# Performance work log

Measured on AMD Instinct MI355X. Metric: run time of the kernel, lower is better.

## Reference

```python
import jax, jax.numpy as jnp
import numpy as np

B, S, D, H = 2, 2048, 1024, 16
HD = D // H               # head_dim = input_size / num_heads
STEPS = 1                 # update_steps_max extra Hopfield update steps
LN_EPS = 1e-5
SCALING = 1.0 / np.sqrt(HD)  # beta = 1/sqrt(head_dim)


def layernorm(x, g, b):
    m = x.mean(-1, keepdims=True)
    v = ((x - m) ** 2).mean(-1, keepdims=True)
    return (x - m) * jax.lax.rsqrt(v + LN_EPS) * g + b


def setup_inputs() -> dict:
    key = jax.random.key(0)
    ks = jax.random.split(key, 9)
    s = 0.02
    f32 = jnp.float32
    return {
        "data": jax.random.normal(ks[0], (B, S, D), f32),
        # affine LayerNorm params (stored / state / projection patterns)
        "g_k": jnp.ones((D,), f32), "b_k": jnp.zeros((D,), f32),
        "g_q": jnp.ones((D,), f32), "b_q": jnp.zeros((D,), f32),
        "g_v": jnp.ones((D,), f32), "b_v": jnp.zeros((D,), f32),
        # in-projections (q/k/v) and out-projection of HopfieldCore
        "Wq": jax.random.normal(ks[1], (D, D), f32) * s, "bq": jnp.zeros((D,), f32),
        "Wk": jax.random.normal(ks[2], (D, D), f32) * s, "bk": jnp.zeros((D,), f32),
        "Wv": jax.random.normal(ks[3], (D, D), f32) * s, "bv": jnp.zeros((D,), f32),
        "Wo": jax.random.normal(ks[4], (D, D), f32) * s, "bo": jnp.zeros((D,), f32),
    }


def reference(data, g_k, b_k, g_q, b_q, g_v, b_v,
              Wq, bq, Wk, bk, Wv, bv, Wo, bo):
    # single input tensor used as stored / state / projection pattern
    xk = layernorm(data, g_k, b_k)   # stored pattern  -> keys
    xq = layernorm(data, g_q, b_q)   # state pattern   -> queries
    xv = layernorm(data, g_v, b_v)   # pattern proj    -> values

    split = lambda t: t.reshape(B, S, H, HD).transpose(0, 2, 1, 3)  # [B,H,S,HD]
    q = split(xq @ Wq + bq)
    k = split(xk @ Wk + bk)
    v = split(xv @ Wv + bv)

    def assoc(q):  # xi = softmax(beta * q K^T)
        return jax.nn.softmax(
            jnp.einsum('bhqd,bhkd->bhqk', q, k) * SCALING, axis=-1)

    xi = assoc(q)
    for _ in range(STEPS):           # iterative Hopfield update: q <- xi K
        q = jnp.einsum('bhqk,bhkd->bhqd', xi, k)
        xi = assoc(q)

    out = jnp.einsum('bhqk,bhkd->bhqd', xi, v)        # retrieve with values
    out = out.transpose(0, 2, 1, 3).reshape(B, S, D)  # merge heads
    return out @ Wo + bo
```

## Files before the change

### kernel.cpp

```cpp
#include <hip/hip_runtime.h>
#include <hip/hip_bf16.h>

#define B_  2
#define S_  2048
#define D_  1024
#define H_  16
#define HD_ 64
#define M_  4096


typedef __attribute__((ext_vector_type(8))) short short8;
typedef __attribute__((ext_vector_type(4))) float f32x4;
typedef __attribute__((ext_vector_type(16))) float f32x16;

#define CE_ 0.1803368801111204f

typedef __attribute__((address_space(1))) const unsigned GU;
typedef __attribute__((address_space(3))) unsigned LU;
static __device__ __forceinline__ void glds16(const void* g, void* l){
  __builtin_amdgcn_global_load_lds((GU*)g, (LU*)l, 16, 0, 0);
}

static __device__ __forceinline__ unsigned short f2bfc(float f){
  union{float f; unsigned u;} c; c.f = f;
  return (unsigned short)((c.u + 0x8000u) >> 16);
}
static __device__ __forceinline__ unsigned pk2bf(float a, float b){
  union{float f; unsigned u;} ca, cb; ca.f=a; cb.f=b;
  return __builtin_amdgcn_perm(cb.u + 0x8000u, ca.u + 0x8000u, 0x07060302u);
}
static __device__ __forceinline__ unsigned pk2bft(float a, float b){
  union{float f; unsigned u;} ca, cb; ca.f=a; cb.f=b;
  return __builtin_amdgcn_perm(cb.u, ca.u, 0x07060302u);
}
static __device__ __forceinline__ short8 mk8(unsigned x0, unsigned x1,
                                             unsigned x2, unsigned x3){
  union{ unsigned u[4]; short8 s; } t;
  t.u[0]=x0; t.u[1]=x1; t.u[2]=x2; t.u[3]=x3; return t.s;
}
static __device__ __forceinline__ void plswap(unsigned &x, unsigned &y){
  auto r = __builtin_amdgcn_permlane32_swap(x, y, false, false);
  x = (unsigned)r[0]; y = (unsigned)r[1];
}

__global__ __launch_bounds__(256) void prep_kernel(
  const float* __restrict__ data,
  const float* __restrict__ Wq, const float* __restrict__ Wk,
  const float* __restrict__ Wv, const float* __restrict__ Wo,
  const float* __restrict__ gq, const float* __restrict__ gk, const float* __restrict__ gv,
  const float* __restrict__ blq, const float* __restrict__ blk, const float* __restrict__ blv,
  const float* __restrict__ bpq, const float* __restrict__ bpk, const float* __restrict__ bpv,
  unsigned short* __restrict__ WT, unsigned short* __restrict__ xhat,
  float* __restrict__ bf)
{
  __shared__ unsigned short tile[64][72];
  __shared__ float red[4][64];
  int bid = blockIdx.x, t = threadIdx.x;
  if (bid < 1024){
    int z = bid >> 8, rem = bid & 255;
    int k0 = (rem>>4)*64, n0 = (rem&15)*64;
    const float* W = (z==0)?Wq:(z==1)?Wk:(z==2)?Wv:Wo;
    const float* g = (z==0)?gq:(z==1)?gk:(z==2)?gv:(const float*)0;
    unsigned short* out = WT + ((size_t)z<<20);
    {
      int kr = t>>2, c16 = (t&3)*16;
      float gs = g ? g[k0+kr]*((z==0)?CE_:1.0f) : 1.0f;
      const float* src = W + (size_t)(k0+kr)*D_ + n0 + c16;
      float4 w0 = *(const float4*)(src);
      float4 w1 = *(const float4*)(src+4);
      float4 w2 = *(const float4*)(src+8);
      float4 w3 = *(const float4*)(src+12);
      unsigned* tp = (unsigned*)&tile[kr][c16];
      tp[0]=pk2bf(w0.x*gs,w0.y*gs); tp[1]=pk2bf(w0.z*gs,w0.w*gs);
      tp[2]=pk2bf(w1.x*gs,w1.y*gs); tp[3]=pk2bf(w1.z*gs,w1.w*gs);
      tp[4]=pk2bf(w2.x*gs,w2.y*gs); tp[5]=pk2bf(w2.z*gs,w2.w*gs);
      tp[6]=pk2bf(w3.x*gs,w3.y*gs); tp[7]=pk2bf(w3.z*gs,w3.w*gs);
    }
    __syncthreads();
    {
      int nr = t>>2, kc = (t&3)*16;
      union { uint4 v[2]; unsigned short u[16]; } st;
      #pragma unroll
      for (int i=0;i<16;i++) st.u[i] = tile[kc+i][nr];
      unsigned short* dst = out + (size_t)(n0+nr)*D_ + k0 + kc;
      *(uint4*)(dst)     = st.v[0];
      *(uint4*)(dst + 8) = st.v[1];
    }
  } else if (bid < 2048){
    int row = (bid-1024)*4 + (t>>6);
    int l = t & 63;
    const float4* xr = (const float4*)(data + (size_t)row*D_);
    float4 v[4];
    float s = 0.f, ss = 0.f;
    #pragma unroll
    for (int i=0;i<4;i++){
      v[i] = xr[l + 64*i];
      s  += v[i].x+v[i].y+v[i].z+v[i].w;
      ss += v[i].x*v[i].x+v[i].y*v[i].y+v[i].z*v[i].z+v[i].w*v[i].w;
    }
    #pragma unroll
    for (int m=1;m<64;m<<=1){ s += __shfl_xor(s, m, 64); ss += __shfl_xor(ss, m, 64); }
    float me = s*(1.0f/D_);
    float var = ss*(1.0f/D_) - me*me;
    float rs = rsqrtf(var + 1e-5f);
    float nm = -me*rs;
    unsigned short* xo = xhat + (size_t)row*D_;
    #pragma unroll
    for (int i=0;i<4;i++){
      uint2 pk;
      pk.x = pk2bf(fmaf(v[i].x,rs,nm), fmaf(v[i].y,rs,nm));
      pk.y = pk2bf(fmaf(v[i].z,rs,nm), fmaf(v[i].w,rs,nm));
      *(uint2*)(xo + 4*l + 256*i) = pk;
    }
  } else {
    int idx = bid - 2048;
    int z = idx >> 4, xb = idx & 15;
    const float* W  = (z==0)?Wq:(z==1)?Wk:Wv;
    const float* bl = (z==0)?blq:(z==1)?blk:blv;
    const float* bp = (z==0)?bpq:(z==1)?bpk:bpv;
    int nl = t & 63, kg = t >> 6;
    int n = xb*64 + nl;
    float acc = 0.f;
    for (int k = kg*256; k < (kg+1)*256; k++)
      acc += bl[k] * W[(size_t)k*D_ + n];
    red[kg][nl] = acc;
    __syncthreads();
    if (t < 64){
      int nn = xb*64 + t;
      float v = red[0][t]+red[1][t]+red[2][t]+red[3][t] + bp[nn];
      bf[z*D_ + nn] = (z==0) ? v*CE_ : v;
    }
  }
}

__global__ __launch_bounds__(256) void gemm_qkv(
  const unsigned short* __restrict__ xhat,
  const unsigned short* __restrict__ WT,
  const float* __restrict__ biasf,
  unsigned short* __restrict__ qv, unsigned short* __restrict__ kb,
  unsigned short* __restrict__ kT, unsigned short* __restrict__ vT)
{
  int z = blockIdx.z;
  const unsigned short* Bt = WT + ((size_t)z<<20);
  const float* bias = biasf + z*D_;
  unsigned short* oN = (z==0)?qv:(z==1)?kb:(unsigned short*)0;
  unsigned short* oT = (z==0)?(unsigned short*)0:(z==1)?kT:vT;

  __shared__ __align__(16) unsigned short As[128*32];
  __shared__ __align__(16) unsigned short Bs[128*32];
  int tid = threadIdx.x, w = tid>>6, l = tid&63;
  int m0 = blockIdx.x*128, n0 = blockIdx.y*128;
  int wr = (w>>1)*64, wc = (w&1)*64;
  int lr = l&15, qd = l>>4;

  const unsigned short* gA = xhat + (size_t)(m0 + w*32 + (l>>2))*D_ + (l&3)*8;
  const unsigned short* gB = Bt   + (size_t)(n0 + w*32 + (l>>2))*D_ + (l&3)*8;
  unsigned short* lA0 = &As[(w*32)*32];
  unsigned short* lA1 = &As[(w*32+16)*32];
  unsigned short* lB0 = &Bs[(w*32)*32];
  unsigned short* lB1 = &Bs[(w*32+16)*32];

  const f32x4 fz = {0.f,0.f,0.f,0.f};
  f32x4 acc[4][4];
  #pragma unroll
  for (int i=0;i<4;i++)
    #pragma unroll
    for (int j=0;j<4;j++) acc[i][j] = fz;

  for (int kk=0; kk<D_; kk+=32){
    __syncthreads();
    glds16(gA + kk,                 lA0);
    glds16(gA + kk + (size_t)16*D_, lA1);
    glds16(gB + kk,                 lB0);
    glds16(gB + kk + (size_t)16*D_, lB1);
    __syncthreads();
    short8 af[4], bfr[4];
    #pragma unroll
    for (int i=0;i<4;i++) af[i]  = *(const short8*)(As + (wr + i*16 + lr)*32 + qd*8);
    #pragma unroll
    for (int j=0;j<4;j++) bfr[j] = *(const short8*)(Bs + (wc + j*16 + lr)*32 + qd*8);
    #pragma unroll
    for (int i=0;i<4;i++)
      #pragma unroll
      for (int j=0;j<4;j++)
        acc[i][j] = __builtin_amdgcn_mfma_f32_16x16x32_bf16(af[i], bfr[j], acc[i][j], 0, 0, 0);
  }

  #pragma unroll
  for (int j=0;j<4;j++){
    int n = n0 + wc + j*16 + lr;
    float bias_n = bias[n];
    #pragma unroll
    for (int i=0;i<4;i++){
      int mb = m0 + wr + i*16 + qd*4;
      float v0 = acc[i][j][0] + bias_n;
      float v1 = acc[i][j][1] + bias_n;
      float v2 = acc[i][j][2] + bias_n;
      float v3 = acc[i][j][3] + bias_n;
      if (oN){
        oN[(size_t)(mb+0)*D_ + n] = f2bfc(v0);
        oN[(size_t)(mb+1)*D_ + n] = f2bfc(v1);
        oN[(size_t)(mb+2)*D_ + n] = f2bfc(v2);
        oN[(size_t)(mb+3)*D_ + n] = f2bfc(v3);
      }
      if (oT){
        int bb = mb >> 11, sI = mb & (S_-1);
        int hh = n >> 6,  dd = n & 63;
        uint2 pk; pk.x = pk2bf(v0, v1); pk.y = pk2bf(v2, v3);
        *(uint2*)(oT + (size_t)((bb*H_ + hh)*HD_ + dd)*S_ + sI) = pk;
      }
    }
  }
}

__global__ __launch_bounds__(256) void gemm_out(
  const unsigned short* __restrict__ A,
  const unsigned short* __restrict__ Bt,
  const float* __restrict__ bo,
  float* __restrict__ Cf)
{
  __shared__ __align__(16) unsigned short As[128*32];
  __shared__ __align__(16) unsigned short Bs[128*32];
  int tid = threadIdx.x, w = tid>>6, l = tid&63;
  int m0 = blockIdx.x*128, n0 = blockIdx.y*128;
  int wr = (w>>1)*64, wc = (w&1)*64;
  int lr = l&15, qd = l>>4;

  const unsigned short* gA = A  + (size_t)(m0 + w*32 + (l>>2))*D_ + (l&3)*8;
  const unsigned short* gB = Bt + (size_t)(n0 + w*32 + (l>>2))*D_ + (l&3)*8;
  unsigned short* lA0 = &As[(w*32)*32];
  unsigned short* lA1 = &As[(w*32+16)*32];
  unsigned short* lB0 = &Bs[(w*32)*32];
  unsigned short* lB1 = &Bs[(w*32+16)*32];

  const f32x4 fz = {0.f,0.f,0.f,0.f};
  f32x4 acc[4][4];
  #pragma unroll
  for (int i=0;i<4;i++)
    #pragma unroll
    for (int j=0;j<4;j++) acc[i][j] = fz;

  for (int kk=0; kk<D_; kk+=32){
    __syncthreads();
    glds16(gA + kk,                 lA0);
    glds16(gA + kk + (size_t)16*D_, lA1);
    glds16(gB + kk,                 lB0);
    glds16(gB + kk + (size_t)16*D_, lB1);
    __syncthreads();
    short8 af[4], bfr[4];
    #pragma unroll
    for (int i=0;i<4;i++) af[i]  = *(const short8*)(As + (wr + i*16 + lr)*32 + qd*8);
    #pragma unroll
    for (int j=0;j<4;j++) bfr[j] = *(const short8*)(Bs + (wc + j*16 + lr)*32 + qd*8);
    #pragma unroll
    for (int i=0;i<4;i++)
      #pragma unroll
      for (int j=0;j<4;j++)
        acc[i][j] = __builtin_amdgcn_mfma_f32_16x16x32_bf16(af[i], bfr[j], acc[i][j], 0, 0, 0);
  }

  #pragma unroll
  for (int j=0;j<4;j++){
    int n = n0 + wc + j*16 + lr;
    float bias_n = bo[n];
    #pragma unroll
    for (int i=0;i<4;i++){
      int mb = m0 + wr + i*16 + qd*4;
      Cf[(size_t)(mb+0)*D_ + n] = acc[i][j][0] + bias_n;
      Cf[(size_t)(mb+1)*D_ + n] = acc[i][j][1] + bias_n;
      Cf[(size_t)(mb+2)*D_ + n] = acc[i][j][2] + bias_n;
      Cf[(size_t)(mb+3)*D_ + n] = acc[i][j][3] + bias_n;
    }
  }
}

__global__ __launch_bounds__(256, 4) void attn_fused(
  unsigned short* __restrict__ QO,
  const unsigned short* __restrict__ K,
  const unsigned short* __restrict__ KT,
  const unsigned short* __restrict__ VT)
{
  int qt = blockIdx.x;
  int h  = blockIdx.y;
  int b  = qt >> 5;
  int bh = b*H_ + h;
  int tid = threadIdx.x, w = tid>>6, l = tid&63;
  int wq = w & 1, wk = w >> 1;
  int lq = l & 31, hi = l >> 5;
  int swzr = (lq & 7) << 3;

  __shared__ __align__(16) unsigned short smem[16384];
  unsigned short* sK = smem;
  unsigned short* sV = smem + 8192;

  const f32x16 fz16 = {0.f,0.f,0.f,0.f,0.f,0.f,0.f,0.f,
                       0.f,0.f,0.f,0.f,0.f,0.f,0.f,0.f};

  const unsigned short* Qb = QO + (size_t)(qt*64 + wq*32 + lq)*D_ + h*64;
  short8 qf[4];
  #pragma unroll
  for (int d=0; d<4; d++) qf[d] = *(const short8*)(Qb + d*16 + hi*8);

  const unsigned short* Khead = K + (size_t)(b*S_)*D_ + h*64;
  const unsigned short* Vh0 = KT + (size_t)bh*HD_*S_;
  const unsigned short* Vh1 = VT + (size_t)bh*HD_*S_;

  int seg = w*4;
  int kcol = ((l&7)*8) ^ (((l>>3)&7)*8);
  const unsigned short* gKb = Khead + (size_t)(seg*8 + (l>>3))*D_ + kcol;
  int vrE = seg*4 + (l>>4);
  int vcE = ((l&15)*8) ^ (((l>>4)&7)*8);
  int vcO = ((l&15)*8) ^ ((((l>>4)+4)&7)*8);

  unsigned short* lK0 = sK + (seg+0)*512;
  unsigned short* lK1 = sK + (seg+1)*512;
  unsigned short* lK2 = sK + (seg+2)*512;
  unsigned short* lK3 = sK + (seg+3)*512;
  unsigned short* lV0 = sV + (seg+0)*512;
  unsigned short* lV1 = sV + (seg+1)*512;
  unsigned short* lV2 = sV + (seg+2)*512;
  unsigned short* lV3 = sV + (seg+3)*512;

  #pragma unroll 1
  for (int phase=0; phase<2; phase++){
    const unsigned short* Vhead = phase ? Vh1 : Vh0;
    const unsigned short* gK  = gKb;
    const unsigned short* gV0 = Vhead + (size_t)(vrE  )*S_ + vcE;
    const unsigned short* gV1 = Vhead + (size_t)(vrE+4)*S_ + vcO;

    f32x16 oacc0 = fz16, oacc1 = fz16;
    float den = 0.f;

    #pragma unroll 1
    for (int ss=0; ss<16; ss++){
      __syncthreads();
      glds16(gK,          lK0);
      glds16(gK +  8*D_,  lK1);
      glds16(gK + 16*D_,  lK2);
      glds16(gK + 24*D_,  lK3);
      glds16(gV0,         lV0);
      glds16(gV1,         lV1);
      glds16(gV0 + 8*S_,  lV2);
      glds16(gV1 + 8*S_,  lV3);
      __syncthreads();
      gK  += 128*D_;
      gV0 += 128;
      gV1 += 128;

      f32x16 sc0 = fz16, sc1 = fz16;
      __builtin_amdgcn_s_setprio(1);
      #pragma unroll
      for (int d4=0; d4<4; d4++){
        int rc = (d4*16 + hi*8) ^ swzr;
        short8 ka0 = *(const short8*)(&sK[(size_t)(wk*64 + lq     )*64 + rc]);
        short8 ka1 = *(const short8*)(&sK[(size_t)(wk*64 + lq + 32)*64 + rc]);
        sc0 = __builtin_amdgcn_mfma_f32_32x32x16_bf16(ka0, qf[d4], sc0, 0,0,0);
        sc1 = __builtin_amdgcn_mfma_f32_32x32x16_bf16(ka1, qf[d4], sc1, 0,0,0);
      }
      __builtin_amdgcn_s_setprio(0);

      float p0[16], p1[16];
      #pragma unroll
      for (int i=0;i<16;i++){
        p0[i] = __builtin_amdgcn_exp2f(sc0[i]);
        p1[i] = __builtin_amdgcn_exp2f(sc1[i]);
      }
      {
        float t0 = ((p0[0]+p0[1])+(p0[2]+p0[3])) + ((p0[4]+p0[5])+(p0[6]+p0[7]));
        float t1 = ((p0[8]+p0[9])+(p0[10]+p0[11])) + ((p0[12]+p0[13])+(p0[14]+p0[15]));
        float t2 = ((p1[0]+p1[1])+(p1[2]+p1[3])) + ((p1[4]+p1[5])+(p1[6]+p1[7]));
        float t3 = ((p1[8]+p1[9])+(p1[10]+p1[11])) + ((p1[12]+p1[13])+(p1[14]+p1[15]));
        den += (t0+t1)+(t2+t3);
      }
      short8 pf[4];
      {
        unsigned a0,a1,b0,b1;
        a0=pk2bft(p0[0],p0[1]);   a1=pk2bft(p0[2],p0[3]);
        b0=pk2bft(p0[4],p0[5]);   b1=pk2bft(p0[6],p0[7]);
        plswap(a0,b0); plswap(a1,b1);
        pf[0] = mk8(a0,a1,b0,b1);
        a0=pk2bft(p0[8],p0[9]);   a1=pk2bft(p0[10],p0[11]);
        b0=pk2bft(p0[12],p0[13]); b1=pk2bft(p0[14],p0[15]);
        plswap(a0,b0); plswap(a1,b1);
        pf[1] = mk8(a0,a1,b0,b1);
        a0=pk2bft(p1[0],p1[1]);   a1=pk2bft(p1[2],p1[3]);
        b0=pk2bft(p1[4],p1[5]);   b1=pk2bft(p1[6],p1[7]);
        plswap(a0,b0); plswap(a1,b1);
        pf[2] = mk8(a0,a1,b0,b1);
        a0=pk2bft(p1[8],p1[9]);   a1=pk2bft(p1[10],p1[11]);
        b0=pk2bft(p1[12],p1[13]); b1=pk2bft(p1[14],p1[15]);
        plswap(a0,b0); plswap(a1,b1);
        pf[3] = mk8(a0,a1,b0,b1);
      }

      __builtin_amdgcn_s_setprio(1);
      #pragma unroll
      for (int ks=0; ks<4; ks++){
        int rc = (wk*64 + ks*16 + hi*8) ^ swzr;
        short8 va0 = *(const short8*)(&sV[(size_t)(lq     )*128 + rc]);
        short8 va1 = *(const short8*)(&sV[(size_t)(lq + 32)*128 + rc]);
        oacc0 = __builtin_amdgcn_mfma_f32_32x32x16_bf16(va0, pf[ks], oacc0, 0,0,0);
        oacc1 = __builtin_amdgcn_mfma_f32_32x32x16_bf16(va1, pf[ks], oacc1, 0,0,0);
      }
      __builtin_amdgcn_s_setprio(0);
    }

    den += __shfl_xor(den, 32, 64);

    float* fb = (float*)smem;
    int cb = wq*2112;
    __syncthreads();
    if (wk==1){
      #pragma unroll
      for (int i=0;i<16;i++){
        fb[cb + i*64 + l]      = oacc0[i];
        fb[cb + (16+i)*64 + l] = oacc1[i];
      }
      fb[cb + 2048 + l] = den;
    }
    __syncthreads();
    if (wk==0){
      #pragma unroll
      for (int i=0;i<16;i++){
        oacc0[i] += fb[cb + i*64 + l];
        oacc1[i] += fb[cb + (16+i)*64 + l];
      }
      den += fb[cb + 2048 + l];
      if (phase==0){
        float iv = CE_ * __builtin_amdgcn_rcpf(den);
        unsigned a0,a1,b0,b1;
        a0=pk2bf(oacc0[0]*iv, oacc0[1]*iv);   a1=pk2bf(oacc0[2]*iv, oacc0[3]*iv);
        b0=pk2bf(oacc0[4]*iv, oacc0[5]*iv);   b1=pk2bf(oacc0[6]*iv, oacc0[7]*iv);
        plswap(a0,b0); plswap(a1,b1);
        qf[0] = mk8(a0,a1,b0,b1);
        a0=pk2bf(oacc0[8]*iv, oacc0[9]*iv);   a1=pk2bf(oacc0[10]*iv, oacc0[11]*iv);
        b0=pk2bf(oacc0[12]*iv, oacc0[13]*iv); b1=pk2bf(oacc0[14]*iv, oacc0[15]*iv);
        plswap(a0,b0); plswap(a1,b1);
        qf[1] = mk8(a0,a1,b0,b1);
        a0=pk2bf(oacc1[0]*iv, oacc1[1]*iv);   a1=pk2bf(oacc1[2]*iv, oacc1[3]*iv);
        b0=pk2bf(oacc1[4]*iv, oacc1[5]*iv);   b1=pk2bf(oacc1[6]*iv, oacc1[7]*iv);
        plswap(a0,b0); plswap(a1,b1);
        qf[2] = mk8(a0,a1,b0,b1);
        a0=pk2bf(oacc1[8]*iv, oacc1[9]*iv);   a1=pk2bf(oacc1[10]*iv, oacc1[11]*iv);
        b0=pk2bf(oacc1[12]*iv, oacc1[13]*iv); b1=pk2bf(oacc1[14]*iv, oacc1[15]*iv);
        plswap(a0,b0); plswap(a1,b1);
        qf[3] = mk8(a0,a1,b0,b1);
        unsigned short* qsh = smem + 12288 + wq*2048;
        #pragma unroll
        for (int d=0; d<4; d++)
          *(short8*)(qsh + d*512 + l*8) = qf[d];
      } else {
        float iv = __builtin_amdgcn_rcpf(den);
        unsigned short* Ob = QO + (size_t)(qt*64 + wq*32 + lq)*D_ + h*64 + hi*4;
        #pragma unroll
        for (int g=0; g<4; g++){
          uint2 pk;
          pk.x = pk2bf(oacc0[4*g+0]*iv, oacc0[4*g+1]*iv);
          pk.y = pk2bf(oacc0[4*g+2]*iv, oacc0[4*g+3]*iv);
          *(uint2*)(Ob + g*8) = pk;
          pk.x = pk2bf(oacc1[4*g+0]*iv, oacc1[4*g+1]*iv);
          pk.y = pk2bf(oacc1[4*g+2]*iv, oacc1[4*g+3]*iv);
          *(uint2*)(Ob + 32 + g*8) = pk;
        }
      }
    }
    __syncthreads();
    if (phase==0 && wk==1){
      unsigned short* qsh = smem + 12288 + wq*2048;
      #pragma unroll
      for (int d=0; d<4; d++)
        qf[d] = *(const short8*)(qsh + d*512 + l*8);
    }
  }
}

extern "C" void kernel_launch(void* const* d_in, const int* in_sizes, int n_in,
                              void* d_out, int out_size, void* d_ws, size_t ws_size,
                              hipStream_t stream){
  const float* data = (const float*)d_in[0];
  const float* g_k  = (const float*)d_in[1];
  const float* b_k  = (const float*)d_in[2];
  const float* g_q  = (const float*)d_in[3];
  const float* b_q  = (const float*)d_in[4];
  const float* g_v  = (const float*)d_in[5];
  const float* b_v  = (const float*)d_in[6];
  const float* Wq   = (const float*)d_in[7];
  const float* bq   = (const float*)d_in[8];
  const float* Wk   = (const float*)d_in[9];
  const float* bk   = (const float*)d_in[10];
  const float* Wv   = (const float*)d_in[11];
  const float* bv   = (const float*)d_in[12];
  const float* Wo   = (const float*)d_in[13];
  const float* bo   = (const float*)d_in[14];
  float* out = (float*)d_out;

  char* ws = (char*)d_ws;
  const size_t MB = (size_t)1<<20;
  unsigned short* q    = (unsigned short*)(ws);
  unsigned short* kb   = (unsigned short*)(ws + 8*MB);
  unsigned short* WT   = (unsigned short*)(ws + 16*MB);
  unsigned short* WTo  = WT + ((size_t)3<<20);
  unsigned short* xhat = (unsigned short*)(ws + 24*MB);
  float*          bfld = (float*)(ws + 32*MB);
  unsigned short* vT   = (unsigned short*)d_out;
  unsigned short* kT   = (unsigned short*)((char*)d_out + 8*MB);

  dim3 gb(256);
  prep_kernel<<<dim3(2096), gb, 0, stream>>>(data,
                                             Wq, Wk, Wv, Wo, g_q, g_k, g_v,
                                             b_q, b_k, b_v, bq, bk, bv,
                                             WT, xhat, bfld);
  gemm_qkv<<<dim3(32,8,3), gb, 0, stream>>>(xhat, WT, bfld, q, kb, kT, vT);
  attn_fused<<<dim3(64, H_), gb, 0, stream>>>(q, kb, kT, vT);
  gemm_out<<<dim3(32,8), gb, 0, stream>>>(q, WTo, bo, out);
}
```

Baseline: 251.9 us.

## Split attention keys across four waves with full query tile per wave

Each of the four waves now owns 32 keys of the 128-key tile and computes scores for all 64 queries, reusing one K fragment for two MFMAs instead of loading two. The PV product likewise has each wave cover its own key slice across all 64 head dims. Partial outputs and denominators from the four waves are then reduced through shared memory in two rounds. This cuts LDS reads of K and V per MFMA and balances epilogue work across waves, but it adds a heavier cross-wave reduction with more barriers and more accumulator registers.

New measurement: 387.2 us. 1.54x slower.

```diff
diff --git a/kernel.cpp b/kernel.cpp
--- a/kernel.cpp
+++ b/kernel.cpp
@@ -11,6 +11,7 @@
 
 typedef __attribute__((ext_vector_type(8))) short short8;
 typedef __attribute__((ext_vector_type(4))) float f32x4;
+typedef __attribute__((ext_vector_type(2))) float f32x2;
 typedef __attribute__((ext_vector_type(16))) float f32x16;
 
 #define CE_ 0.1803368801111204f
@@ -41,6 +42,14 @@
 static __device__ __forceinline__ void plswap(unsigned &x, unsigned &y){
   auto r = __builtin_amdgcn_permlane32_swap(x, y, false, false);
   x = (unsigned)r[0]; y = (unsigned)r[1];
+}
+static __device__ __forceinline__ short8 conv8(const float* s, float iv){
+  unsigned a0 = pk2bf(s[0]*iv, s[1]*iv);
+  unsigned a1 = pk2bf(s[2]*iv, s[3]*iv);
+  unsigned b0 = pk2bf(s[4]*iv, s[5]*iv);
+  unsigned b1 = pk2bf(s[6]*iv, s[7]*iv);
+  plswap(a0,b0); plswap(a1,b1);
+  return mk8(a0,a1,b0,b1);
 }
 
 __global__ __launch_bounds__(256) void prep_kernel(
@@ -285,21 +294,26 @@
   int b  = qt >> 5;
   int bh = b*H_ + h;
   int tid = threadIdx.x, w = tid>>6, l = tid&63;
-  int wq = w & 1, wk = w >> 1;
   int lq = l & 31, hi = l >> 5;
   int swzr = (lq & 7) << 3;
-
-  __shared__ __align__(16) unsigned short smem[16384];
+  int dr_ = w >> 1, rh_ = w & 1;
+
+  __shared__ __align__(16) unsigned short smem[17408];
   unsigned short* sK = smem;
   unsigned short* sV = smem + 8192;
+  float* dn = (float*)(smem + 16384);
 
   const f32x16 fz16 = {0.f,0.f,0.f,0.f,0.f,0.f,0.f,0.f,
                        0.f,0.f,0.f,0.f,0.f,0.f,0.f,0.f};
-
-  const unsigned short* Qb = QO + (size_t)(qt*64 + wq*32 + lq)*D_ + h*64;
-  short8 qf[4];
+  const f32x2 fz2 = {0.f,0.f};
+
+  const unsigned short* Qb = QO + (size_t)(qt*64 + lq)*D_ + h*64;
+  short8 qf[2][4];
   #pragma unroll
-  for (int d=0; d<4; d++) qf[d] = *(const short8*)(Qb + d*16 + hi*8);
+  for (int qc=0; qc<2; qc++)
+    #pragma unroll
+    for (int d=0; d<4; d++)
+      qf[qc][d] = *(const short8*)(Qb + (size_t)qc*32*D_ + d*16 + hi*8);
 
   const unsigned short* Khead = K + (size_t)(b*S_)*D_ + h*64;
   const unsigned short* Vh0 = KT + (size_t)bh*HD_*S_;
@@ -328,8 +342,9 @@
     const unsigned short* gV0 = Vhead + (size_t)(vrE  )*S_ + vcE;
     const unsigned short* gV1 = Vhead + (size_t)(vrE+4)*S_ + vcO;
 
-    f32x16 oacc0 = fz16, oacc1 = fz16;
-    float den = 0.f;
+    f32x16 oacc[2][2];
+    oacc[0][0]=fz16; oacc[0][1]=fz16; oacc[1][0]=fz16; oacc[1][1]=fz16;
+    f32x2 dq0 = fz2, dq1 = fz2;
 
     #pragma unroll 1
     for (int ss=0; ss<16; ss++){
@@ -351,125 +366,121 @@
       __builtin_amdgcn_s_setprio(1);
       #pragma unroll
       for (int d4=0; d4<4; d4++){
-        int rc = (d4*16 + hi*8) ^ swzr;
-        short8 ka0 = *(const short8*)(&sK[(size_t)(wk*64 + lq     )*64 + rc]);
-        short8 ka1 = *(const short8*)(&sK[(size_t)(wk*64 + lq + 32)*64 + rc]);
-        sc0 = __builtin_amdgcn_mfma_f32_32x32x16_bf16(ka0, qf[d4], sc0, 0,0,0);
-        sc1 = __builtin_amdgcn_mfma_f32_32x32x16_bf16(ka1, qf[d4], sc1, 0,0,0);
+        short8 ka = *(const short8*)(&sK[(size_t)(w*32 + lq)*64 + ((d4*16 + hi*8) ^ swzr)]);
+        sc0 = __builtin_amdgcn_mfma_f32_32x32x16_bf16(ka, qf[0][d4], sc0, 0,0,0);
+        sc1 = __builtin_amdgcn_mfma_f32_32x32x16_bf16(ka, qf[1][d4], sc1, 0,0,0);
       }
       __builtin_amdgcn_s_setprio(0);
 
-      float p0[16], p1[16];
       #pragma unroll
       for (int i=0;i<16;i++){
-        p0[i] = __builtin_amdgcn_exp2f(sc0[i]);
-        p1[i] = __builtin_amdgcn_exp2f(sc1[i]);
-      }
-      {
-        float t0 = ((p0[0]+p0[1])+(p0[2]+p0[3])) + ((p0[4]+p0[5])+(p0[6]+p0[7]));
-        float t1 = ((p0[8]+p0[9])+(p0[10]+p0[11])) + ((p0[12]+p0[13])+(p0[14]+p0[15]));
-        float t2 = ((p1[0]+p1[1])+(p1[2]+p1[3])) + ((p1[4]+p1[5])+(p1[6]+p1[7]));
-        float t3 = ((p1[8]+p1[9])+(p1[10]+p1[11])) + ((p1[12]+p1[13])+(p1[14]+p1[15]));
-        den += (t0+t1)+(t2+t3);
-      }
-      short8 pf[4];
+        sc0[i] = __builtin_amdgcn_exp2f(sc0[i]);
+        sc1[i] = __builtin_amdgcn_exp2f(sc1[i]);
+      }
+      #pragma unroll
+      for (int i=0;i<16;i+=2){
+        dq0 += (f32x2){sc0[i], sc0[i+1]};
+        dq1 += (f32x2){sc1[i], sc1[i+1]};
+      }
+
+      short8 pf0[2], pf1[2];
       {
         unsigned a0,a1,b0,b1;
-        a0=pk2bft(p0[0],p0[1]);   a1=pk2bft(p0[2],p0[3]);
-        b0=pk2bft(p0[4],p0[5]);   b1=pk2bft(p0[6],p0[7]);
+        a0=pk2bft(sc0[0],sc0[1]);   a1=pk2bft(sc0[2],sc0[3]);
+        b0=pk2bft(sc0[4],sc0[5]);   b1=pk2bft(sc0[6],sc0[7]);
         plswap(a0,b0); plswap(a1,b1);
-        pf[0] = mk8(a0,a1,b0,b1);
-        a0=pk2bft(p0[8],p0[9]);   a1=pk2bft(p0[10],p0[11]);
-        b0=pk2bft(p0[12],p0[13]); b1=pk2bft(p0[14],p0[15]);
+        pf0[0] = mk8(a0,a1,b0,b1);
+        a0=pk2bft(sc0[8],sc0[9]);   a1=pk2bft(sc0[10],sc0[11]);
+        b0=pk2bft(sc0[12],sc0[13]); b1=pk2bft(sc0[14],sc0[15]);
         plswap(a0,b0); plswap(a1,b1);
-        pf[1] = mk8(a0,a1,b0,b1);
-        a0=pk2bft(p1[0],p1[1]);   a1=pk2bft(p1[2],p1[3]);
-        b0=pk2bft(p1[4],p1[5]);   b1=pk2bft(p1[6],p1[7]);
+        pf0[1] = mk8(a0,a1,b0,b1);
+        a0=pk2bft(sc1[0],sc1[1]);   a1=pk2bft(sc1[2],sc1[3]);
+        b0=pk2bft(sc1[4],sc1[5]);   b1=pk2bft(sc1[6],sc1[7]);
         plswap(a0,b0); plswap(a1,b1);
-        pf[2] = mk8(a0,a1,b0,b1);
-        a0=pk2bft(p1[8],p1[9]);   a1=pk2bft(p1[10],p1[11]);
-        b0=pk2bft(p1[12],p1[13]); b1=pk2bft(p1[14],p1[15]);
+        pf1[0] = mk8(a0,a1,b0,b1);
+        a0=pk2bft(sc1[8],sc1[9]);   a1=pk2bft(sc1[10],sc1[11]);
+        b0=pk2bft(sc1[12],sc1[13]); b1=pk2bft(sc1[14],sc1[15]);
         plswap(a0,b0); plswap(a1,b1);
-        pf[3] = mk8(a0,a1,b0,b1);
+        pf1[1] = mk8(a0,a1,b0,b1);
       }
 
       __builtin_amdgcn_s_setprio(1);
       #pragma unroll
-      for (int ks=0; ks<4; ks++){
-        int rc = (wk*64 + ks*16 + hi*8) ^ swzr;
-        short8 va0 = *(const short8*)(&sV[(size_t)(lq     )*128 + rc]);
-        short8 va1 = *(const short8*)(&sV[(size_t)(lq + 32)*128 + rc]);
-        oacc0 = __builtin_amdgcn_mfma_f32_32x32x16_bf16(va0, pf[ks], oacc0, 0,0,0);
-        oacc1 = __builtin_amdgcn_mfma_f32_32x32x16_bf16(va1, pf[ks], oacc1, 0,0,0);
+      for (int dr=0; dr<2; dr++){
+        #pragma unroll
+        for (int ks=0; ks<2; ks++){
+          short8 va = *(const short8*)(&sV[(size_t)(dr*32 + lq)*128 + ((w*32 + ks*16 + hi*8) ^ swzr)]);
+          oacc[0][dr] = __builtin_amdgcn_mfma_f32_32x32x16_bf16(va, pf0[ks], oacc[0][dr], 0,0,0);
+          oacc[1][dr] = __builtin_amdgcn_mfma_f32_32x32x16_bf16(va, pf1[ks], oacc[1][dr], 0,0,0);
+        }
       }
       __builtin_amdgcn_s_setprio(0);
     }
 
-    den += __shfl_xor(den, 32, 64);
+    float den0 = dq0.x + dq0.y; den0 += __shfl_xor(den0, 32, 64);
+    float den1 = dq1.x + dq1.y; den1 += __shfl_xor(den1, 32, 64);
 
     float* fb = (float*)smem;
-    int cb = wq*2112;
-    __syncthreads();
-    if (wk==1){
-      #pragma unroll
-      for (int i=0;i<16;i++){
-        fb[cb + i*64 + l]      = oacc0[i];
-        fb[cb + (16+i)*64 + l] = oacc1[i];
-      }
-      fb[cb + 2048 + l] = den;
-    }
-    __syncthreads();
-    if (wk==0){
-      #pragma unroll
-      for (int i=0;i<16;i++){
-        oacc0[i] += fb[cb + i*64 + l];
-        oacc1[i] += fb[cb + (16+i)*64 + l];
-      }
-      den += fb[cb + 2048 + l];
-      if (phase==0){
-        float iv = CE_ * __builtin_amdgcn_rcpf(den);
-        unsigned a0,a1,b0,b1;
-        a0=pk2bf(oacc0[0]*iv, oacc0[1]*iv);   a1=pk2bf(oacc0[2]*iv, oacc0[3]*iv);
-        b0=pk2bf(oacc0[4]*iv, oacc0[5]*iv);   b1=pk2bf(oacc0[6]*iv, oacc0[7]*iv);
-        plswap(a0,b0); plswap(a1,b1);
-        qf[0] = mk8(a0,a1,b0,b1);
-        a0=pk2bf(oacc0[8]*iv, oacc0[9]*iv);   a1=pk2bf(oacc0[10]*iv, oacc0[11]*iv);
-        b0=pk2bf(oacc0[12]*iv, oacc0[13]*iv); b1=pk2bf(oacc0[14]*iv, oacc0[15]*iv);
-        plswap(a0,b0); plswap(a1,b1);
-        qf[1] = mk8(a0,a1,b0,b1);
-        a0=pk2bf(oacc1[0]*iv, oacc1[1]*iv);   a1=pk2bf(oacc1[2]*iv, oacc1[3]*iv);
-        b0=pk2bf(oacc1[4]*iv, oacc1[5]*iv);   b1=pk2bf(oacc1[6]*iv, oacc1[7]*iv);
-        plswap(a0,b0); plswap(a1,b1);
-        qf[2] = mk8(a0,a1,b0,b1);
-        a0=pk2bf(oacc1[8]*iv, oacc1[9]*iv);   a1=pk2bf(oacc1[10]*iv, oacc1[11]*iv);
-        b0=pk2bf(oacc1[12]*iv, oacc1[13]*iv); b1=pk2bf(oacc1[14]*iv, oacc1[15]*iv);
-        plswap(a0,b0); plswap(a1,b1);
-        qf[3] = mk8(a0,a1,b0,b1);
-        unsigned short* qsh = smem + 12288 + wq*2048;
+    __syncthreads();
+    #pragma unroll
+    for (int dr=0; dr<2; dr++)
+      #pragma unroll
+      for (int g=0; g<16; g++)
+        fb[w*2048 + (dr*16+g)*64 + l] = oacc[0][dr][g];
+    dn[w*64 + l]       = den0;
+    dn[256 + w*64 + l] = den1;
+    __syncthreads();
+    float s0[8], dt0, dt1;
+    {
+      #pragma unroll
+      for (int j=0;j<8;j++){
+        int off = (dr_*16 + rh_*8 + j)*64 + l;
+        s0[j] = (fb[off] + fb[2048+off]) + (fb[4096+off] + fb[6144+off]);
+      }
+      dt0 = (dn[l] + dn[64+l]) + (dn[128+l] + dn[192+l]);
+      dt1 = (dn[256+l] + dn[320+l]) + (dn[384+l] + dn[448+l]);
+    }
+    __syncthreads();
+    #pragma unroll
+    for (int dr=0; dr<2; dr++)
+      #pragma unroll
+      for (int g=0; g<16; g++)
+        fb[w*2048 + (dr*16+g)*64 + l] = oacc[1][dr][g];
+    __syncthreads();
+    float s1[8];
+    #pragma unroll
+    for (int j=0;j<8;j++){
+      int off = (dr_*16 + rh_*8 + j)*64 + l;
+      s1[j] = (fb[off] + fb[2048+off]) + (fb[4096+off] + fb[6144+off]);
+    }
+
+    if (phase==0){
+      short8 f0 = conv8(s0, CE_ * __builtin_amdgcn_rcpf(dt0));
+      short8 f1 = conv8(s1, CE_ * __builtin_amdgcn_rcpf(dt1));
+      __syncthreads();
+      *(short8*)(smem + (size_t)(0*4 + w)*512 + l*8) = f0;
+      *(short8*)(smem + (size_t)(1*4 + w)*512 + l*8) = f1;
+      __syncthreads();
+      #pragma unroll
+      for (int qc=0; qc<2; qc++)
         #pragma unroll
-        for (int d=0; d<4; d++)
-          *(short8*)(qsh + d*512 + l*8) = qf[d];
-      } else {
-        float iv = __builtin_amdgcn_rcpf(den);
-        unsigned short* Ob = QO + (size_t)(qt*64 + wq*32 + lq)*D_ + h*64 + hi*4;
-        #pragma unroll
-        for (int g=0; g<4; g++){
-          uint2 pk;
-          pk.x = pk2bf(oacc0[4*g+0]*iv, oacc0[4*g+1]*iv);
-          pk.y = pk2bf(oacc0[4*g+2]*iv, oacc0[4*g+3]*iv);
-          *(uint2*)(Ob + g*8) = pk;
-          pk.x = pk2bf(oacc1[4*g+0]*iv, oacc1[4*g+1]*iv);
-          pk.y = pk2bf(oacc1[4*g+2]*iv, oacc1[4*g+3]*iv);
-          *(uint2*)(Ob + 32 + g*8) = pk;
-        }
-      }
-    }
-    __syncthreads();
-    if (phase==0 && wk==1){
-      unsigned short* qsh = smem + 12288 + wq*2048;
-      #pragma unroll
-      for (int d=0; d<4; d++)
-        qf[d] = *(const short8*)(qsh + d*512 + l*8);
+        for (int ds=0; ds<4; ds++)
+          qf[qc][ds] = *(const short8*)(smem + (size_t)(qc*4 + ds)*512 + l*8);
+    } else {
+      float iv0 = __builtin_amdgcn_rcpf(dt0);
+      float iv1 = __builtin_amdgcn_rcpf(dt1);
+      unsigned short* Ob0 = QO + (size_t)(qt*64 + 0*32 + lq)*D_ + h*64 + dr_*32 + hi*4;
+      unsigned short* Ob1 = QO + (size_t)(qt*64 + 1*32 + lq)*D_ + h*64 + dr_*32 + hi*4;
+      #pragma unroll
+      for (int gg=0; gg<2; gg++){
+        uint2 pk;
+        pk.x = pk2bf(s0[gg*4+0]*iv0, s0[gg*4+1]*iv0);
+        pk.y = pk2bf(s0[gg*4+2]*iv0, s0[gg*4+3]*iv0);
+        *(uint2*)(Ob0 + (rh_*2+gg)*8) = pk;
+        pk.x = pk2bf(s1[gg*4+0]*iv1, s1[gg*4+1]*iv1);
+        pk.y = pk2bf(s1[gg*4+2]*iv1, s1[gg*4+3]*iv1);
+        *(uint2*)(Ob1 + (rh_*2+gg)*8) = pk;
+      }
     }
   }
 }
```

## Double-buffer K/V tiles with prefetch across phases in fused attention

Applied to the files above, without the earlier changes.

Replaces the single-buffered 128-key tile loop, which synced twice per step, with a 64-key double-buffered pipeline. The next tile's K and V (or K^T/V^T) loads are issued before computing on the current buffer, and the prefetch runs across the boundary between the two phases. This leaves one barrier per step and aims to hide global-to-LDS latency behind the MFMA work. In exchange each step carries half the MFMA work, the loop runs twice as many iterations, and the reduction scratch layout in LDS grows and moves.

New measurement: 254.6 us. Within noise of the previous version (+1.1%).

```diff
diff --git a/kernel.cpp b/kernel.cpp
--- a/kernel.cpp
+++ b/kernel.cpp
@@ -11,6 +11,7 @@
 
 typedef __attribute__((ext_vector_type(8))) short short8;
 typedef __attribute__((ext_vector_type(4))) float f32x4;
+typedef __attribute__((ext_vector_type(2))) float f32x2;
 typedef __attribute__((ext_vector_type(16))) float f32x16;
 
 #define CE_ 0.1803368801111204f
@@ -41,6 +42,22 @@
 static __device__ __forceinline__ void plswap(unsigned &x, unsigned &y){
   auto r = __builtin_amdgcn_permlane32_swap(x, y, false, false);
   x = (unsigned)r[0]; y = (unsigned)r[1];
+}
+static __device__ __forceinline__ short8 conv8a(const f32x16& v, float iv){
+  unsigned a0 = pk2bf(v[0]*iv, v[1]*iv);
+  unsigned a1 = pk2bf(v[2]*iv, v[3]*iv);
+  unsigned b0 = pk2bf(v[4]*iv, v[5]*iv);
+  unsigned b1 = pk2bf(v[6]*iv, v[7]*iv);
+  plswap(a0,b0); plswap(a1,b1);
+  return mk8(a0,a1,b0,b1);
+}
+static __device__ __forceinline__ short8 conv8b(const f32x16& v, float iv){
+  unsigned a0 = pk2bf(v[8]*iv,  v[9]*iv);
+  unsigned a1 = pk2bf(v[10]*iv, v[11]*iv);
+  unsigned b0 = pk2bf(v[12]*iv, v[13]*iv);
+  unsigned b1 = pk2bf(v[14]*iv, v[15]*iv);
+  plswap(a0,b0); plswap(a1,b1);
+  return mk8(a0,a1,b0,b1);
 }
 
 __global__ __launch_bounds__(256) void prep_kernel(
@@ -289,9 +306,7 @@
   int lq = l & 31, hi = l >> 5;
   int swzr = (lq & 7) << 3;
 
-  __shared__ __align__(16) unsigned short smem[16384];
-  unsigned short* sK = smem;
-  unsigned short* sV = smem + 8192;
+  __shared__ __align__(16) unsigned short smem[17408];
 
   const f32x16 fz16 = {0.f,0.f,0.f,0.f,0.f,0.f,0.f,0.f,
                        0.f,0.f,0.f,0.f,0.f,0.f,0.f,0.f};
@@ -305,147 +320,114 @@
   const unsigned short* Vh0 = KT + (size_t)bh*HD_*S_;
   const unsigned short* Vh1 = VT + (size_t)bh*HD_*S_;
 
-  int seg = w*4;
-  int kcol = ((l&7)*8) ^ (((l>>3)&7)*8);
-  const unsigned short* gKb = Khead + (size_t)(seg*8 + (l>>3))*D_ + kcol;
-  int vrE = seg*4 + (l>>4);
-  int vcE = ((l&15)*8) ^ (((l>>4)&7)*8);
-  int vcO = ((l&15)*8) ^ ((((l>>4)+4)&7)*8);
-
-  unsigned short* lK0 = sK + (seg+0)*512;
-  unsigned short* lK1 = sK + (seg+1)*512;
-  unsigned short* lK2 = sK + (seg+2)*512;
-  unsigned short* lK3 = sK + (seg+3)*512;
-  unsigned short* lV0 = sV + (seg+0)*512;
-  unsigned short* lV1 = sV + (seg+1)*512;
-  unsigned short* lV2 = sV + (seg+2)*512;
-  unsigned short* lV3 = sV + (seg+3)*512;
+  int seg0 = w*2;
+  int lr8 = l>>3;
+  int swzs = ((l&7)*8) ^ (lr8*8);
+  const unsigned short* gKs  = Khead + (size_t)(seg0*8 + lr8)*D_ + swzs;
+  const unsigned short* gV0s = Vh0 + (size_t)(seg0*8 + lr8)*S_ + swzs;
+  const unsigned short* gV1s = Vh1 + (size_t)(seg0*8 + lr8)*S_ + swzs;
+  int dK0 = seg0*512 + l*8;
+  int dV0 = 4096 + seg0*512 + l*8;
+
+  glds16(gKs,         smem + dK0);
+  glds16(gKs + 8*D_,  smem + dK0 + 512);
+  glds16(gV0s,        smem + dV0);
+  glds16(gV0s + 8*S_, smem + dV0 + 512);
+  __syncthreads();
 
   #pragma unroll 1
   for (int phase=0; phase<2; phase++){
-    const unsigned short* Vhead = phase ? Vh1 : Vh0;
-    const unsigned short* gK  = gKb;
-    const unsigned short* gV0 = Vhead + (size_t)(vrE  )*S_ + vcE;
-    const unsigned short* gV1 = Vhead + (size_t)(vrE+4)*S_ + vcO;
-
-    f32x16 oacc0 = fz16, oacc1 = fz16;
-    float den = 0.f;
+    f32x16 oacc[2]; oacc[0]=fz16; oacc[1]=fz16;
+    f32x2 dq = {0.f,0.f};
 
     #pragma unroll 1
-    for (int ss=0; ss<16; ss++){
-      __syncthreads();
-      glds16(gK,          lK0);
-      glds16(gK +  8*D_,  lK1);
-      glds16(gK + 16*D_,  lK2);
-      glds16(gK + 24*D_,  lK3);
-      glds16(gV0,         lV0);
-      glds16(gV1,         lV1);
-      glds16(gV0 + 8*S_,  lV2);
-      glds16(gV1 + 8*S_,  lV3);
-      __syncthreads();
-      gK  += 128*D_;
-      gV0 += 128;
-      gV1 += 128;
-
-      f32x16 sc0 = fz16, sc1 = fz16;
+    for (int ss=0; ss<32; ss++){
+      int t = phase*32 + ss;
+      if (t < 63){
+        int tn = t + 1;
+        int tt = tn & 31;
+        unsigned short* bb = smem + ((tn&1) ? 8192 : 0);
+        const unsigned short* gk = gKs + (size_t)tt*64*D_;
+        const unsigned short* gv = ((tn >= 32) ? gV1s : gV0s) + tt*64;
+        glds16(gk,         bb + dK0);
+        glds16(gk + 8*D_,  bb + dK0 + 512);
+        glds16(gv,         bb + dV0);
+        glds16(gv + 8*S_,  bb + dV0 + 512);
+      }
+      __builtin_amdgcn_sched_barrier(0);
+
+      const unsigned short* sKc = smem + ((t&1) ? 8192 : 0);
+      const unsigned short* sVc = sKc + 4096;
+
+      f32x16 sc = fz16;
       __builtin_amdgcn_s_setprio(1);
       #pragma unroll
       for (int d4=0; d4<4; d4++){
-        int rc = (d4*16 + hi*8) ^ swzr;
-        short8 ka0 = *(const short8*)(&sK[(size_t)(wk*64 + lq     )*64 + rc]);
-        short8 ka1 = *(const short8*)(&sK[(size_t)(wk*64 + lq + 32)*64 + rc]);
-        sc0 = __builtin_amdgcn_mfma_f32_32x32x16_bf16(ka0, qf[d4], sc0, 0,0,0);
-        sc1 = __builtin_amdgcn_mfma_f32_32x32x16_bf16(ka1, qf[d4], sc1, 0,0,0);
+        short8 ka = *(const short8*)(sKc + (size_t)(wk*32 + lq)*64 + ((d4*16 + hi*8) ^ swzr));
+        sc = __builtin_amdgcn_mfma_f32_32x32x16_bf16(ka, qf[d4], sc, 0,0,0);
       }
       __builtin_amdgcn_s_setprio(0);
 
-      float p0[16], p1[16];
-      #pragma unroll
-      for (int i=0;i<16;i++){
-        p0[i] = __builtin_amdgcn_exp2f(sc0[i]);
-        p1[i] = __builtin_amdgcn_exp2f(sc1[i]);
-      }
-      {
-        float t0 = ((p0[0]+p0[1])+(p0[2]+p0[3])) + ((p0[4]+p0[5])+(p0[6]+p0[7]));
-        float t1 = ((p0[8]+p0[9])+(p0[10]+p0[11])) + ((p0[12]+p0[13])+(p0[14]+p0[15]));
-        float t2 = ((p1[0]+p1[1])+(p1[2]+p1[3])) + ((p1[4]+p1[5])+(p1[6]+p1[7]));
-        float t3 = ((p1[8]+p1[9])+(p1[10]+p1[11])) + ((p1[12]+p1[13])+(p1[14]+p1[15]));
-        den += (t0+t1)+(t2+t3);
-      }
-      short8 pf[4];
+      #pragma unroll
+      for (int i=0;i<16;i++) sc[i] = __builtin_amdgcn_exp2f(sc[i]);
+      #pragma unroll
+      for (int i=0;i<16;i+=2) dq += (f32x2){sc[i], sc[i+1]};
+
+      short8 pf[2];
       {
         unsigned a0,a1,b0,b1;
-        a0=pk2bft(p0[0],p0[1]);   a1=pk2bft(p0[2],p0[3]);
-        b0=pk2bft(p0[4],p0[5]);   b1=pk2bft(p0[6],p0[7]);
+        a0=pk2bft(sc[0],sc[1]);   a1=pk2bft(sc[2],sc[3]);
+        b0=pk2bft(sc[4],sc[5]);   b1=pk2bft(sc[6],sc[7]);
         plswap(a0,b0); plswap(a1,b1);
         pf[0] = mk8(a0,a1,b0,b1);
-        a0=pk2bft(p0[8],p0[9]);   a1=pk2bft(p0[10],p0[11]);
-        b0=pk2bft(p0[12],p0[13]); b1=pk2bft(p0[14],p0[15]);
+        a0=pk2bft(sc[8],sc[9]);   a1=pk2bft(sc[10],sc[11]);
+        b0=pk2bft(sc[12],sc[13]); b1=pk2bft(sc[14],sc[15]);
         plswap(a0,b0); plswap(a1,b1);
         pf[1] = mk8(a0,a1,b0,b1);
-        a0=pk2bft(p1[0],p1[1]);   a1=pk2bft(p1[2],p1[3]);
-        b0=pk2bft(p1[4],p1[5]);   b1=pk2bft(p1[6],p1[7]);
-        plswap(a0,b0); plswap(a1,b1);
-        pf[2] = mk8(a0,a1,b0,b1);
-        a0=pk2bft(p1[8],p1[9]);   a1=pk2bft(p1[10],p1[11]);
-        b0=pk2bft(p1[12],p1[13]); b1=pk2bft(p1[14],p1[15]);
-        plswap(a0,b0); plswap(a1,b1);
-        pf[3] = mk8(a0,a1,b0,b1);
       }
 
       __builtin_amdgcn_s_setprio(1);
       #pragma unroll
-      for (int ks=0; ks<4; ks++){
-        int rc = (wk*64 + ks*16 + hi*8) ^ swzr;
-        short8 va0 = *(const short8*)(&sV[(size_t)(lq     )*128 + rc]);
-        short8 va1 = *(const short8*)(&sV[(size_t)(lq + 32)*128 + rc]);
-        oacc0 = __builtin_amdgcn_mfma_f32_32x32x16_bf16(va0, pf[ks], oacc0, 0,0,0);
-        oacc1 = __builtin_amdgcn_mfma_f32_32x32x16_bf16(va1, pf[ks], oacc1, 0,0,0);
+      for (int dr=0; dr<2; dr++){
+        #pragma unroll
+        for (int ks=0; ks<2; ks++){
+          short8 va = *(const short8*)(sVc + (size_t)(dr*32 + lq)*64 + ((wk*32 + ks*16 + hi*8) ^ swzr));
+          oacc[dr] = __builtin_amdgcn_mfma_f32_32x32x16_bf16(va, pf[ks], oacc[dr], 0,0,0);
+        }
       }
       __builtin_amdgcn_s_setprio(0);
-    }
-
+
+      __syncthreads();
+    }
+
+    float den = dq.x + dq.y;
     den += __shfl_xor(den, 32, 64);
 
-    float* fb = (float*)smem;
-    int cb = wq*2112;
-    __syncthreads();
+    float* fb  = (float*)(smem + 8192);
+    float* dnp = (float*)(smem + 16384);
     if (wk==1){
       #pragma unroll
-      for (int i=0;i<16;i++){
-        fb[cb + i*64 + l]      = oacc0[i];
-        fb[cb + (16+i)*64 + l] = oacc1[i];
-      }
-      fb[cb + 2048 + l] = den;
+      for (int dr=0; dr<2; dr++)
+        #pragma unroll
+        for (int g=0; g<16; g++)
+          fb[wq*2048 + (dr*16+g)*64 + l] = oacc[dr][g];
+      dnp[wq*64 + l] = den;
     }
     __syncthreads();
     if (wk==0){
       #pragma unroll
-      for (int i=0;i<16;i++){
-        oacc0[i] += fb[cb + i*64 + l];
-        oacc1[i] += fb[cb + (16+i)*64 + l];
-      }
-      den += fb[cb + 2048 + l];
+      for (int dr=0; dr<2; dr++)
+        #pragma unroll
+        for (int g=0; g<16; g++)
+          oacc[dr][g] += fb[wq*2048 + (dr*16+g)*64 + l];
+      den += dnp[wq*64 + l];
       if (phase==0){
         float iv = CE_ * __builtin_amdgcn_rcpf(den);
-        unsigned a0,a1,b0,b1;
-        a0=pk2bf(oacc0[0]*iv, oacc0[1]*iv);   a1=pk2bf(oacc0[2]*iv, oacc0[3]*iv);
-        b0=pk2bf(oacc0[4]*iv, oacc0[5]*iv);   b1=pk2bf(oacc0[6]*iv, oacc0[7]*iv);
-        plswap(a0,b0); plswap(a1,b1);
-        qf[0] = mk8(a0,a1,b0,b1);
-        a0=pk2bf(oacc0[8]*iv, oacc0[9]*iv);   a1=pk2bf(oacc0[10]*iv, oacc0[11]*iv);
-        b0=pk2bf(oacc0[12]*iv, oacc0[13]*iv); b1=pk2bf(oacc0[14]*iv, oacc0[15]*iv);
-        plswap(a0,b0); plswap(a1,b1);
-        qf[1] = mk8(a0,a1,b0,b1);
-        a0=pk2bf(oacc1[0]*iv, oacc1[1]*iv);   a1=pk2bf(oacc1[2]*iv, oacc1[3]*iv);
-        b0=pk2bf(oacc1[4]*iv, oacc1[5]*iv);   b1=pk2bf(oacc1[6]*iv, oacc1[7]*iv);
-        plswap(a0,b0); plswap(a1,b1);
-        qf[2] = mk8(a0,a1,b0,b1);
-        a0=pk2bf(oacc1[8]*iv, oacc1[9]*iv);   a1=pk2bf(oacc1[10]*iv, oacc1[11]*iv);
-        b0=pk2bf(oacc1[12]*iv, oacc1[13]*iv); b1=pk2bf(oacc1[14]*iv, oacc1[15]*iv);
-        plswap(a0,b0); plswap(a1,b1);
-        qf[3] = mk8(a0,a1,b0,b1);
-        unsigned short* qsh = smem + 12288 + wq*2048;
+        qf[0] = conv8a(oacc[0], iv);
+        qf[1] = conv8b(oacc[0], iv);
+        qf[2] = conv8a(oacc[1], iv);
+        qf[3] = conv8b(oacc[1], iv);
+        unsigned short* qsh = smem + 8192 + wq*6144;
         #pragma unroll
         for (int d=0; d<4; d++)
           *(short8*)(qsh + d*512 + l*8) = qf[d];
@@ -455,22 +437,23 @@
         #pragma unroll
         for (int g=0; g<4; g++){
           uint2 pk;
-          pk.x = pk2bf(oacc0[4*g+0]*iv, oacc0[4*g+1]*iv);
-          pk.y = pk2bf(oacc0[4*g+2]*iv, oacc0[4*g+3]*iv);
+          pk.x = pk2bf(oacc[0][4*g+0]*iv, oacc[0][4*g+1]*iv);
+          pk.y = pk2bf(oacc[0][4*g+2]*iv, oacc[0][4*g+3]*iv);
           *(uint2*)(Ob + g*8) = pk;
-          pk.x = pk2bf(oacc1[4*g+0]*iv, oacc1[4*g+1]*iv);
-          pk.y = pk2bf(oacc1[4*g+2]*iv, oacc1[4*g+3]*iv);
+          pk.x = pk2bf(oacc[1][4*g+0]*iv, oacc[1][4*g+1]*iv);
+          pk.y = pk2bf(oacc[1][4*g+2]*iv, oacc[1][4*g+3]*iv);
           *(uint2*)(Ob + 32 + g*8) = pk;
         }
       }
     }
     __syncthreads();
     if (phase==0 && wk==1){
-      unsigned short* qsh = smem + 12288 + wq*2048;
+      unsigned short* qsh = smem + 8192 + wq*6144;
       #pragma unroll
       for (int d=0; d<4; d++)
         qf[d] = *(const short8*)(qsh + d*512 + l*8);
     }
+    __syncthreads();
   }
 }
 
```
